# Optimization experiments

Hardware: AMD Instinct MI355X
Metric: run time of the kernel (lower is better)

## Reference

```python
import jax, jax.numpy as jnp
import numpy as np

CAPACITY_FACTOR = 1.0
MIN_CAPACITY = 4


def setup_inputs() -> dict:
    key = jax.random.key(0)
    ks = jax.random.split(key, 4)
    B, S, D, E, F = 4, 2048, 1024, 16, 4096
    hidden_states = jax.random.normal(ks[0], (B, S, D), dtype=jnp.float32)
    wg = jax.random.normal(ks[1], (D, E), dtype=jnp.float32) * 0.02
    w1 = jax.random.normal(ks[2], (E, D, F), dtype=jnp.float32) * (1.0 / np.sqrt(D))
    b1 = jnp.zeros((E, F), dtype=jnp.float32)
    w2 = jax.random.normal(ks[3], (E, F, D), dtype=jnp.float32) * (1.0 / np.sqrt(F))
    b2 = jnp.zeros((E, D), dtype=jnp.float32)
    return {"hidden_states": hidden_states, "wg": wg, "w1": w1, "b1": b1, "w2": w2, "b2": b2}


def reference(hidden_states, wg, w1, b1, w2, b2):
    B, S, D = hidden_states.shape
    x = hidden_states.reshape(-1, D)                      # [T, D] tokens
    T = x.shape[0]
    E = wg.shape[1]
    capacity = max(int(np.ceil(T / E * CAPACITY_FACTOR)), MIN_CAPACITY)  # static

    # ---- TopKGate (k=1, no noise, no RTS) ----
    logits = x @ wg                                       # [T, E]
    gates = jax.nn.softmax(logits, axis=-1)
    idx1 = jnp.argmax(gates, axis=1)                      # [T]
    mask1 = jax.nn.one_hot(idx1, E, dtype=gates.dtype)    # [T, E]
    exp_counts = jnp.sum(mask1, axis=0).astype(jnp.int32) # per-expert token counts

    # load-balancing aux loss
    me = jnp.mean(gates, axis=0)
    ce = jnp.mean(mask1, axis=0)
    l_aux = jnp.sum(me * ce) * E

    # slot assignment within each expert, drop overflow tokens
    locations1 = jnp.cumsum(mask1, axis=0) - 1.0          # [T, E]
    mask1 = mask1 * (locations1 < capacity).astype(gates.dtype)
    locations1_s = jnp.sum(locations1 * mask1, axis=1).astype(jnp.int32)  # [T]
    gates1 = gates * mask1                                # [T, E] gate prob of kept assignment

    loc_oh = jax.nn.one_hot(locations1_s, capacity, dtype=gates.dtype)    # [T, C]
    combine = jnp.einsum('te,tc->tec', gates1, loc_oh)    # [T, E, C]
    dispatch = (combine > 0).astype(x.dtype)              # [T, E, C]

    # ---- dispatch -> grouped expert FFN -> combine ----
    disp = jnp.einsum('tec,td->ecd', dispatch, x)         # [E, C, D]
    h = jax.nn.gelu(jnp.einsum('ecd,edf->ecf', disp, w1) + b1[:, None, :])
    eo = jnp.einsum('ecf,efd->ecd', h, w2) + b2[:, None, :]  # [E, C, D]
    out = jnp.einsum('tec,ecd->td', combine, eo).reshape(B, S, D)
    return out, l_aux, exp_counts
```

## Files before the change

### kernel.cpp

```cpp
#include <hip/hip_runtime.h>

typedef unsigned short u16;
typedef unsigned int   u32;
typedef unsigned long long u64;
typedef __attribute__((ext_vector_type(8))) __bf16 bf16x8;
typedef __attribute__((ext_vector_type(4))) float  f32x4;

#define TOK 8192
#define DIM 1024
#define NE  16
#define NF  4096
#define CAP 512

__device__ __forceinline__ u16 f2bf(float f) {
    u32 u = __float_as_uint(f);
    u32 r = (u + 0x7FFFu + ((u >> 16) & 1u)) >> 16;
    return (u16)r;
}

__device__ __forceinline__ float gelu_tanh(float x) {
    float u = 0.7978845608028654f * (x + 0.044715f * x * x * x);
    float t = __expf(-2.f * fabsf(u));
    float th = (1.f - t) / (1.f + t);
    th = (u < 0.f) ? -th : th;
    return 0.5f * x * (1.f + th);
}

__device__ __forceinline__ void gld16(const void* g, void* l) {
    __builtin_amdgcn_global_load_lds(
        (const __attribute__((address_space(1))) void*)g,
        (__attribute__((address_space(3))) void*)l, 16, 0, 0);
}

__global__ void moe_init(float* me_sums) {
    if (threadIdx.x < NE) me_sums[threadIdx.x] = 0.f;
}

__global__ void moe_wgT(const float* __restrict__ wg, float* __restrict__ wgT) {
    int i = blockIdx.x * 256 + threadIdx.x;
    int d = i >> 4, e = i & 15;
    wgT[(size_t)e * DIM + d] = wg[i];
}

__global__ void moe_gate(const float* __restrict__ x, const float* __restrict__ wgT,
                         int* __restrict__ eidx, float* __restrict__ gp,
                         float* __restrict__ me_sums) {
    __shared__ float lme[NE];
    const int tid = threadIdx.x;
    if (tid < NE) lme[tid] = 0.f;
    __syncthreads();
    const int tok = blockIdx.x * 16 + (tid >> 4);
    const int e   = tid & 15;
    const float4* xp = (const float4*)(x + (size_t)tok * DIM);
    const float4* wp = (const float4*)(wgT + (size_t)e * DIM);
    float acc = 0.f;
#pragma unroll 4
    for (int i = 0; i < DIM / 4; ++i) {
        float4 a = xp[i], b = wp[i];
        acc = fmaf(a.x, b.x, acc); acc = fmaf(a.y, b.y, acc);
        acc = fmaf(a.z, b.z, acc); acc = fmaf(a.w, b.w, acc);
    }
    float mx = acc;
    for (int off = 8; off; off >>= 1) mx = fmaxf(mx, __shfl_xor(mx, off, 16));
    float ex = __expf(acc - mx);
    float sum = ex;
    for (int off = 8; off; off >>= 1) sum += __shfl_xor(sum, off, 16);
    float p = ex / sum;
    atomicAdd(&lme[e], p);
    float bv = acc; int bi = e;
    for (int off = 8; off; off >>= 1) {
        float ov = __shfl_xor(bv, off, 16);
        int   oi = __shfl_xor(bi, off, 16);
        if (ov > bv || (ov == bv && oi < bi)) { bv = ov; bi = oi; }
    }
    float pw = __shfl(p, bi, 16);
    if (e == 0) { eidx[tok] = bi; gp[tok] = pw; }
    __syncthreads();
    if (tid < NE) atomicAdd(&me_sums[tid], lme[tid]);
}

__global__ void moe_scan(const int* __restrict__ eidx, const float* __restrict__ me_sums,
                         int* __restrict__ slot, int* __restrict__ tos,
                         float* __restrict__ tail ) {
    __shared__ int wcnt[16][16];
    __shared__ int base[16];
    const int tid = threadIdx.x, wid = tid >> 6, lane = tid & 63;
    if (tid < 16) base[tid] = 0;
    for (int i = tid; i < NE * CAP; i += 1024) tos[i] = -1;
    __syncthreads();
    const u64 below = ((u64)1 << lane) - 1;
    for (int chunk = 0; chunk < TOK / 1024; ++chunk) {
        int t = chunk * 1024 + tid;
        int e = eidx[t];
        int rank = 0;
#pragma unroll
        for (int ex = 0; ex < 16; ++ex) {
            u64 m = __ballot(e == ex);
            if (e == ex)    rank = __popcll(m & below);
            if (lane == ex) wcnt[wid][ex] = __popcll(m);
        }
        __syncthreads();
        int pre = base[e];
        for (int w = 0; w < wid; ++w) pre += wcnt[w][e];
        int s = pre + rank;
        slot[t] = s;
        if (s < CAP) tos[e * CAP + s] = t;
        __syncthreads();
        if (tid < 16) {
            int tot = 0;
            for (int w = 0; w < 16; ++w) tot += wcnt[w][tid];
            base[tid] += tot;
        }
        __syncthreads();
    }
    if (tid == 0) {
        float laux = 0.f;
        for (int e2 = 0; e2 < 16; ++e2) {
            float me = me_sums[e2] / (float)TOK;
            float ce = (float)base[e2] / (float)TOK;
            laux += me * ce;
        }
        tail[0] = laux * (float)NE;
    }
    if (tid < 16) tail[1 + tid] = (float)base[tid];
}

__global__ void moe_gather(const float* __restrict__ x, const int* __restrict__ tos,
                           u16* __restrict__ Xg) {
    const int s = blockIdx.x, tid = threadIdx.x;
    const int t = tos[s];
    float4 v = make_float4(0.f, 0.f, 0.f, 0.f);
    if (t >= 0) v = *(const float4*)(x + (size_t)t * DIM + tid * 4);
    u32 lo = (u32)f2bf(v.x) | ((u32)f2bf(v.y) << 16);
    u32 hi = (u32)f2bf(v.z) | ((u32)f2bf(v.w) << 16);
    *(uint2*)(Xg + (size_t)s * DIM + tid * 4) = make_uint2(lo, hi);
}

__global__ void moe_zero_dropped(const int* __restrict__ slot, float* __restrict__ out) {
    const int t = blockIdx.x;
    if (slot[t] < CAP) return;
    *(float4*)(out + (size_t)t * DIM + threadIdx.x * 4) = make_float4(0.f, 0.f, 0.f, 0.f);
}

__global__ void moe_convT(const float* __restrict__ src, u16* __restrict__ dst,
                          int R, int C) {
    __shared__ float tile[64][65];
    int b = blockIdx.x;
    const int tilesC = C >> 6, tilesR = R >> 6;
    int tc = b % tilesC; b /= tilesC;
    int tr = b % tilesR; int e = b / tilesR;
    const float* S = src + ((size_t)e * R + tr * 64) * C + tc * 64;
    const int tid = threadIdx.x;
    const int rr = tid >> 4, cc = (tid & 15) * 4;
#pragma unroll
    for (int i = 0; i < 4; ++i) {
        float4 v = *(const float4*)(S + (size_t)(rr + i * 16) * C + cc);
        tile[rr + i * 16][cc + 0] = v.x; tile[rr + i * 16][cc + 1] = v.y;
        tile[rr + i * 16][cc + 2] = v.z; tile[rr + i * 16][cc + 3] = v.w;
    }
    __syncthreads();
    const int c = tid >> 2, r0 = (tid & 3) * 16;
    u16 tmp[16];
#pragma unroll
    for (int k = 0; k < 16; ++k) tmp[k] = f2bf(tile[r0 + k][c]);
    u16* D = dst + ((size_t)e * C + tc * 64 + c) * R + tr * 64 + r0;
    uint4 w0 = make_uint4((u32)tmp[0] | ((u32)tmp[1] << 16), (u32)tmp[2] | ((u32)tmp[3] << 16),
                          (u32)tmp[4] | ((u32)tmp[5] << 16), (u32)tmp[6] | ((u32)tmp[7] << 16));
    uint4 w1 = make_uint4((u32)tmp[8] | ((u32)tmp[9] << 16), (u32)tmp[10] | ((u32)tmp[11] << 16),
                          (u32)tmp[12] | ((u32)tmp[13] << 16), (u32)tmp[14] | ((u32)tmp[15] << 16));
    *(uint4*)(D) = w0;
    *(uint4*)(D + 8) = w1;
}

__global__ __launch_bounds__(256) void moe_gemm1(const u16* __restrict__ Xg,
                                                 const u16* __restrict__ W1t,
                                                 const float* __restrict__ b1,
                                                 u16* __restrict__ H) {
    __shared__ alignas(16) u16 Als[2][4096];
    __shared__ alignas(16) u16 Bls[2][4096];
    const int tid = threadIdx.x, wave = tid >> 6, lane = tid & 63;
    const int e  = blockIdx.z;
    const int bm = e * 4 + blockIdx.y;
    const int bn = blockIdx.x;
    const int r4  = lane >> 2;
    const int gch = (lane & 3) ^ ((lane >> 3) & 3);
    const u16* aS = Xg + (size_t)(bm * 128 + wave * 32 + r4) * DIM + gch * 8;
    const u16* bS = W1t + (size_t)e * NF * DIM
                  + (size_t)(bn * 128 + wave * 32 + r4) * DIM + gch * 8;
    u16* aD0 = &Als[0][wave * 1024]; u16* aD1 = &Als[1][wave * 1024];
    u16* bD0 = &Bls[0][wave * 1024]; u16* bD1 = &Bls[1][wave * 1024];
    f32x4 acc[4][4] = {};
    const int wm = wave & 1, wn = wave >> 1;
    const int fr = lane & 15, fq = lane >> 4;
    const int rdoff = fr * 32 + (fq ^ ((fr >> 1) & 3)) * 8;

#define STAGE1(AD, BD, K) do { \
        gld16(aS + (K), AD); gld16(aS + (K) + 16 * DIM, (AD) + 512); \
        gld16(bS + (K), BD); gld16(bS + (K) + 16 * DIM, (BD) + 512); } while (0)
#define COMP1(AB, BB) do { \
        bf16x8 aF[4], bF[4]; \
        _Pragma("unroll") for (int i = 0; i < 4; ++i) \
            aF[i] = *(const bf16x8*)(const void*)((AB) + (wm * 64 + i * 16) * 32 + rdoff); \
        _Pragma("unroll") for (int j = 0; j < 4; ++j) \
            bF[j] = *(const bf16x8*)(const void*)((BB) + (wn * 64 + j * 16) * 32 + rdoff); \
        _Pragma("unroll") for (int i = 0; i < 4; ++i) \
        _Pragma("unroll") for (int j = 0; j < 4; ++j) \
            acc[i][j] = __builtin_amdgcn_mfma_f32_16x16x32_bf16(aF[i], bF[j], acc[i][j], 0, 0, 0); \
        } while (0)

    STAGE1(aD0, bD0, 0);
    for (int k0 = 0; k0 < DIM; k0 += 64) {
        __syncthreads();
        if (k0 + 32 < DIM) STAGE1(aD1, bD1, k0 + 32);
        COMP1(&Als[0][0], &Bls[0][0]);
        __syncthreads();
        if (k0 + 64 < DIM) STAGE1(aD0, bD0, k0 + 64);
        COMP1(&Als[1][0], &Bls[1][0]);
    }
#undef STAGE1
#undef COMP1

    const int mBase = bm * 128 + wm * 64;
    const int nBase = bn * 128 + wn * 64;
#pragma unroll
    for (int j = 0; j < 4; ++j) {
        const int f = nBase + j * 16 + fr;
        const float bias = b1[e * NF + f];
#pragma unroll
        for (int i = 0; i < 4; ++i) {
            const int m0 = mBase + i * 16 + fq * 4;
#pragma unroll
            for (int r = 0; r < 4; ++r) {
                float v = acc[i][j][r] + bias;
                H[(size_t)(m0 + r) * NF + f] = f2bf(gelu_tanh(v));
            }
        }
    }
}

__global__ __launch_bounds__(256) void moe_gemm2(const u16* __restrict__ H,
                                                 const u16* __restrict__ W2t,
                                                 const float* __restrict__ b2,
                                                 const int* __restrict__ tos,
                                                 const float* __restrict__ gp,
                                                 float* __restrict__ out) {
    __shared__ alignas(16) u16 Als[2][4096];
    __shared__ alignas(16) u16 Bls[2][2048];
    const int tid = threadIdx.x, wave = tid >> 6, lane = tid & 63;
    const int e  = blockIdx.z;
    const int bm = e * 4 + blockIdx.y;
    const int bn = blockIdx.x;
    const int r4  = lane >> 2;
    const int gch = (lane & 3) ^ ((lane >> 3) & 3);
    const u16* aS = H + (size_t)(bm * 128 + wave * 32 + r4) * NF + gch * 8;
    const u16* bS = W2t + (size_t)e * DIM * NF
                  + (size_t)(bn * 64 + wave * 16 + r4) * NF + gch * 8;
    u16* aD0 = &Als[0][wave * 1024]; u16* aD1 = &Als[1][wave * 1024];
    u16* bD0 = &Bls[0][wave * 512];  u16* bD1 = &Bls[1][wave * 512];
    f32x4 acc[4][2] = {};
    const int wm = wave & 1, wn = wave >> 1;
    const int fr = lane & 15, fq = lane >> 4;
    const int rdoff = fr * 32 + (fq ^ ((fr >> 1) & 3)) * 8;

#define STAGE2(AD, BD, K) do { \
        gld16(aS + (K), AD); gld16(aS + (K) + 16 * NF, (AD) + 512); \
        gld16(bS + (K), BD); } while (0)
#define COMP2(AB, BB) do { \
        bf16x8 aF[4], bF[2]; \
        _Pragma("unroll") for (int i = 0; i < 4; ++i) \
            aF[i] = *(const bf16x8*)(const void*)((AB) + (wm * 64 + i * 16) * 32 + rdoff); \
        _Pragma("unroll") for (int j = 0; j < 2; ++j) \
            bF[j] = *(const bf16x8*)(const void*)((BB) + (wn * 32 + j * 16) * 32 + rdoff); \
        _Pragma("unroll") for (int i = 0; i < 4; ++i) \
        _Pragma("unroll") for (int j = 0; j < 2; ++j) \
            acc[i][j] = __builtin_amdgcn_mfma_f32_16x16x32_bf16(aF[i], bF[j], acc[i][j], 0, 0, 0); \
        } while (0)

    STAGE2(aD0, bD0, 0);
    for (int k0 = 0; k0 < NF; k0 += 64) {
        __syncthreads();
        if (k0 + 32 < NF) STAGE2(aD1, bD1, k0 + 32);
        COMP2(&Als[0][0], &Bls[0][0]);
        __syncthreads();
        if (k0 + 64 < NF) STAGE2(aD0, bD0, k0 + 64);
        COMP2(&Als[1][0], &Bls[1][0]);
    }
#undef STAGE2
#undef COMP2

    const int mBase = bm * 128 + wm * 64;
    const int nBase = bn * 64 + wn * 32;
#pragma unroll
    for (int i = 0; i < 4; ++i) {
#pragma unroll
        for (int r = 0; r < 4; ++r) {
            const int m = mBase + i * 16 + fq * 4 + r;
            const int t = tos[m];
            if (t < 0) continue;
            const float g = gp[t];
#pragma unroll
            for (int j = 0; j < 2; ++j) {
                const int d = nBase + j * 16 + fr;
                out[(size_t)t * DIM + d] = g * (acc[i][j][r] + b2[e * DIM + d]);
            }
        }
    }
}

extern "C" void kernel_launch(void* const* d_in, const int* in_sizes, int n_in,
                              void* d_out, int out_size, void* d_ws, size_t ws_size,
                              hipStream_t stream) {
    const float* x  = (const float*)d_in[0];
    const float* wg = (const float*)d_in[1];
    const float* w1 = (const float*)d_in[2];
    const float* b1 = (const float*)d_in[3];
    const float* w2 = (const float*)d_in[4];
    const float* b2 = (const float*)d_in[5];
    float* out = (float*)d_out;

    char* ws = (char*)d_ws;
    const size_t WBF_OFF = 0;
    const size_t XG_OFF  = WBF_OFF + (size_t)NE * NF * DIM * 2;
    const size_t H_OFF   = XG_OFF + (size_t)TOK * DIM * 2;
    const size_t SM_OFF  = H_OFF + (size_t)TOK * NF * 2;
    u16* Wbf = (u16*)(ws + WBF_OFF);
    u16* Xg  = (u16*)(ws + XG_OFF);
    u16* H   = (u16*)(ws + H_OFF);
    int*   eidx = (int*)(ws + SM_OFF);
    float* gp   = (float*)(ws + SM_OFF + 32768);
    int*   slot = (int*)(ws + SM_OFF + 65536);
    int*   tos  = (int*)(ws + SM_OFF + 98304);
    float* me   = (float*)(ws + SM_OFF + 131072);
    float* wgT  = (float*)(ws + SM_OFF + 131072 + 128);

    float* tail = out + (size_t)TOK * DIM;

    moe_init<<<1, 64, 0, stream>>>(me);
    moe_wgT<<<64, 256, 0, stream>>>(wg, wgT);
    moe_gate<<<TOK / 16, 256, 0, stream>>>(x, wgT, eidx, gp, me);
    moe_scan<<<1, 1024, 0, stream>>>(eidx, me, slot, tos, tail);
    moe_gather<<<NE * CAP, 256, 0, stream>>>(x, tos, Xg);
    moe_zero_dropped<<<TOK, 256, 0, stream>>>(slot, out);
    moe_convT<<<NE * (DIM / 64) * (NF / 64), 256, 0, stream>>>(w1, Wbf, DIM, NF);
    moe_gemm1<<<dim3(NF / 128, 4, NE), 256, 0, stream>>>(Xg, Wbf, b1, H);
    moe_convT<<<NE * (NF / 64) * (DIM / 64), 256, 0, stream>>>(w2, Wbf, NF, DIM);
    moe_gemm2<<<dim3(DIM / 64, 4, NE), 256, 0, stream>>>(H, Wbf, b2, tos, gp, out);
}
```

Before: 942.8 us.

## Remap GEMM blocks per XCD by expert and enlarge gemm2 N tile

Both expert GEMMs switch from a 3D grid to a flat 1D grid. The block index is decoded so each of the 8 XCDs handles two whole experts, which keeps each expert's weights local to one L2. gemm2 also grows its N tile from 64 to 128 with a 4x4 MFMA accumulator per wave, matching gemm1. This gives more reuse of the A tile and half as many blocks, at the cost of more registers and LDS per block and lower parallelism for gemm2 (512 blocks).

```diff
diff --git a/kernel.cpp b/kernel.cpp
--- a/kernel.cpp
+++ b/kernel.cpp
@@ -76,7 +76,7 @@
     float pw = __shfl(p, bi, 16);
     if (e == 0) { eidx[tok] = bi; gp[tok] = pw; }
     __syncthreads();
-    if (tid < NE) atomicAdd(&me_sums[tid], lme[tid]);
+    if (tid < 16) atomicAdd(&me_sums[tid], lme[tid]);
 }
 
 __global__ void moe_scan(const int* __restrict__ eidx, const float* __restrict__ me_sums,
@@ -179,9 +179,14 @@
     __shared__ alignas(16) u16 Als[2][4096];
     __shared__ alignas(16) u16 Bls[2][4096];
     const int tid = threadIdx.x, wave = tid >> 6, lane = tid & 63;
-    const int e  = blockIdx.z;
-    const int bm = e * 4 + blockIdx.y;
-    const int bn = blockIdx.x;
+    const int flat = blockIdx.x;
+    const int xcd  = flat & 7;
+    const int slot = flat >> 3;
+    const int e    = xcd * 2 + (slot >> 7);
+    const int tile = slot & 127;
+    const int bmL  = tile & 3;
+    const int bn   = tile >> 2;
+    const int bm   = e * 4 + bmL;
     const int r4  = lane >> 2;
     const int gch = (lane & 3) ^ ((lane >> 3) & 3);
     const u16* aS = Xg + (size_t)(bm * 128 + wave * 32 + r4) * DIM + gch * 8;
@@ -245,34 +250,39 @@
                                                  const float* __restrict__ gp,
                                                  float* __restrict__ out) {
     __shared__ alignas(16) u16 Als[2][4096];
-    __shared__ alignas(16) u16 Bls[2][2048];
+    __shared__ alignas(16) u16 Bls[2][4096];
     const int tid = threadIdx.x, wave = tid >> 6, lane = tid & 63;
-    const int e  = blockIdx.z;
-    const int bm = e * 4 + blockIdx.y;
-    const int bn = blockIdx.x;
+    const int flat = blockIdx.x;
+    const int xcd  = flat & 7;
+    const int slot = flat >> 3;
+    const int e    = xcd * 2 + (slot >> 5);
+    const int tile = slot & 31;
+    const int bmL  = tile & 3;
+    const int bn   = tile >> 2;
+    const int bm   = e * 4 + bmL;
     const int r4  = lane >> 2;
     const int gch = (lane & 3) ^ ((lane >> 3) & 3);
     const u16* aS = H + (size_t)(bm * 128 + wave * 32 + r4) * NF + gch * 8;
     const u16* bS = W2t + (size_t)e * DIM * NF
-                  + (size_t)(bn * 64 + wave * 16 + r4) * NF + gch * 8;
+                  + (size_t)(bn * 128 + wave * 32 + r4) * NF + gch * 8;
     u16* aD0 = &Als[0][wave * 1024]; u16* aD1 = &Als[1][wave * 1024];
-    u16* bD0 = &Bls[0][wave * 512];  u16* bD1 = &Bls[1][wave * 512];
-    f32x4 acc[4][2] = {};
+    u16* bD0 = &Bls[0][wave * 1024]; u16* bD1 = &Bls[1][wave * 1024];
+    f32x4 acc[4][4] = {};
     const int wm = wave & 1, wn = wave >> 1;
     const int fr = lane & 15, fq = lane >> 4;
     const int rdoff = fr * 32 + (fq ^ ((fr >> 1) & 3)) * 8;
 
 #define STAGE2(AD, BD, K) do { \
         gld16(aS + (K), AD); gld16(aS + (K) + 16 * NF, (AD) + 512); \
-        gld16(bS + (K), BD); } while (0)
+        gld16(bS + (K), BD); gld16(bS + (K) + 16 * NF, (BD) + 512); } while (0)
 #define COMP2(AB, BB) do { \
-        bf16x8 aF[4], bF[2]; \
+        bf16x8 aF[4], bF[4]; \
         _Pragma("unroll") for (int i = 0; i < 4; ++i) \
             aF[i] = *(const bf16x8*)(const void*)((AB) + (wm * 64 + i * 16) * 32 + rdoff); \
-        _Pragma("unroll") for (int j = 0; j < 2; ++j) \
-            bF[j] = *(const bf16x8*)(const void*)((BB) + (wn * 32 + j * 16) * 32 + rdoff); \
+        _Pragma("unroll") for (int j = 0; j < 4; ++j) \
+            bF[j] = *(const bf16x8*)(const void*)((BB) + (wn * 64 + j * 16) * 32 + rdoff); \
         _Pragma("unroll") for (int i = 0; i < 4; ++i) \
-        _Pragma("unroll") for (int j = 0; j < 2; ++j) \
+        _Pragma("unroll") for (int j = 0; j < 4; ++j) \
             acc[i][j] = __builtin_amdgcn_mfma_f32_16x16x32_bf16(aF[i], bF[j], acc[i][j], 0, 0, 0); \
         } while (0)
 
@@ -289,7 +299,7 @@
 #undef COMP2
 
     const int mBase = bm * 128 + wm * 64;
-    const int nBase = bn * 64 + wn * 32;
+    const int nBase = bn * 128 + wn * 64;
 #pragma unroll
     for (int i = 0; i < 4; ++i) {
 #pragma unroll
@@ -299,7 +309,7 @@
             if (t < 0) continue;
             const float g = gp[t];
 #pragma unroll
-            for (int j = 0; j < 2; ++j) {
+            for (int j = 0; j < 4; ++j) {
                 const int d = nBase + j * 16 + fr;
                 out[(size_t)t * DIM + d] = g * (acc[i][j][r] + b2[e * DIM + d]);
             }
@@ -342,7 +352,7 @@
     moe_gather<<<NE * CAP, 256, 0, stream>>>(x, tos, Xg);
     moe_zero_dropped<<<TOK, 256, 0, stream>>>(slot, out);
     moe_convT<<<NE * (DIM / 64) * (NF / 64), 256, 0, stream>>>(w1, Wbf, DIM, NF);
-    moe_gemm1<<<dim3(NF / 128, 4, NE), 256, 0, stream>>>(Xg, Wbf, b1, H);
+    moe_gemm1<<<2048, 256, 0, stream>>>(Xg, Wbf, b1, H);
     moe_convT<<<NE * (NF / 64) * (DIM / 64), 256, 0, stream>>>(w2, Wbf, NF, DIM);
-    moe_gemm2<<<dim3(DIM / 64, 4, NE), 256, 0, stream>>>(H, Wbf, b2, tos, gp, out);
-}
+    moe_gemm2<<<512, 256, 0, stream>>>(H, Wbf, b2, tos, gp, out);
+}
```

Result: no change. 932.4 us (-1.1%).
